# Kernel optimization log

Measured on AMD Instinct MI355X. Metric: run time of the kernel, lower is better.

The kernel has to match this reference:

```python
import jax, jax.numpy as jnp
import numpy as np

N = 10000      # num nodes
R = 16         # num relations
NB = 30        # num bases (hardcoded in source: num_bases=30)
E = 160000     # num edges
IN, HID, OUT = 256, 256, 128


def rgcn_conv(x, src, dst, etype, basis, comp, root, bias):
    """PyG RGCNConv with basis decomposition, aggr='mean' (per relation), root weight + bias."""
    # relation weights from basis decomposition: W_r = sum_b comp[r,b] * basis[b]
    W = jnp.einsum('rb,bio->rio', comp, basis)            # [R, in, out]
    xw = jnp.einsum('ni,rio->rno', x, W)                  # [R, N, out]
    msg = xw[etype, src]                                  # [E, out] gather per edge
    # per-(dst, relation) mean aggregation, then sum over relations
    seg = dst * R + etype                                 # combined segment key
    cnt = jax.ops.segment_sum(jnp.ones((msg.shape[0],), msg.dtype), seg, num_segments=N * R)
    msg = msg / jnp.maximum(cnt[seg], 1.0)[:, None]       # zero-degree -> 0 (matches scatter-mean)
    agg = jax.ops.segment_sum(msg, dst, num_segments=N)   # [N, out]
    return agg + x @ root + bias


def setup_inputs() -> dict:
    key = jax.random.key(0)
    ks = jax.random.split(key, 11)
    g = lambda k, shape, s: jax.random.normal(k, shape, jnp.float32) * s
    s1 = (2.0 / (IN + HID)) ** 0.5
    s2 = (2.0 / (HID + OUT)) ** 0.5
    return dict(
        x=g(ks[0], (N, IN), 1.0),
        edge_index=jax.random.randint(ks[1], (2, E), 0, N),
        edge_type=jax.random.randint(ks[2], (E,), 0, R),
        basis1=g(ks[3], (NB, IN, HID), s1),
        comp1=g(ks[4], (R, NB), 1.0 / NB ** 0.5),
        root1=g(ks[5], (IN, HID), s1),
        bias1=jnp.zeros((HID,), jnp.float32),
        basis2=g(ks[6], (NB, HID, OUT), s2),
        comp2=g(ks[7], (R, NB), 1.0 / NB ** 0.5),
        root2=g(ks[8], (HID, OUT), s2),
        bias2=jnp.zeros((OUT,), jnp.float32),
    )


def reference(x, edge_index, edge_type, basis1, comp1, root1, bias1,
              basis2, comp2, root2, bias2):
    src, dst = edge_index[0], edge_index[1]
    h = jax.nn.relu(rgcn_conv(x, src, dst, edge_type, basis1, comp1, root1, bias1))
    return rgcn_conv(h, src, dst, edge_type, basis2, comp2, root2, bias2)
```

## Files before the change

### kernel.cpp

```cpp
#include <hip/hip_runtime.h>
#include <hip/hip_bf16.h>

#define NN 10000
#define MP 10112
#define RR 16
#define NBASE 30
#define EE 160000
#define HIDF 256
#define OUTF 128
#define NSEG (NN * RR)

typedef __attribute__((ext_vector_type(8))) short bf16x8;
typedef __attribute__((ext_vector_type(4))) short s16x4;
typedef __attribute__((ext_vector_type(4))) float f32x4;

static __device__ __forceinline__ short f2bf(float f) {
    union { float f; unsigned u; } v; v.f = f;
    unsigned r = v.u + 0x7FFFu + ((v.u >> 16) & 1u);
    return (short)(r >> 16);
}
static __device__ __forceinline__ float bf2f(short s) {
    union { unsigned u; float f; } v;
    v.u = ((unsigned)(unsigned short)s) << 16;
    return v.f;
}
static __device__ __forceinline__ void gl16(const short* g, short* l) {
    __builtin_amdgcn_global_load_lds((const __attribute__((address_space(1))) void*)g,
                                     (__attribute__((address_space(3))) void*)l, 16, 0, 0);
}

template <int OUT>
__global__ void wtr_k(const float* __restrict__ basis, const float* __restrict__ comp,
                      const float* __restrict__ root, short* __restrict__ WT) {
    __shared__ short t[32][34];
    const int i0 = blockIdx.x * 32, n0 = blockIdx.y * 32;
    const int r = n0 / OUT, o0 = n0 % OUT;
    const int tx = threadIdx.x & 31, ty = threadIdx.x >> 5;
    #pragma unroll
    for (int dy = 0; dy < 32; dy += 8) {
        const int i = i0 + ty + dy, o = o0 + tx;
        float v;
        if (r < RR) {
            float s = 0.f;
            #pragma unroll
            for (int b = 0; b < NBASE; b++)
                s += comp[r * NBASE + b] * basis[((long)b * 256 + i) * OUT + o];
            v = s;
        } else {
            v = root[(long)i * OUT + o];
        }
        t[ty + dy][tx] = f2bf(v);
    }
    __syncthreads();
    #pragma unroll
    for (int dy = 0; dy < 32; dy += 8)
        WT[(long)(n0 + ty + dy) * 256 + i0 + tx] = t[tx][ty + dy];
}

__global__ void count_k(const int* __restrict__ dst, const int* __restrict__ et,
                        int* __restrict__ cnt) {
    int e = blockIdx.x * 256 + threadIdx.x;
    if (e < EE) atomicAdd(&cnt[dst[e] * RR + et[e]], 1);
}

__global__ void scan1_k(const int* __restrict__ cnt, int* __restrict__ incl,
                        int* __restrict__ bsum) {
    __shared__ int s[256];
    int i = blockIdx.x * 256 + threadIdx.x;
    int v = (i < NSEG) ? cnt[i] : 0;
    s[threadIdx.x] = v;
    __syncthreads();
    for (int off = 1; off < 256; off <<= 1) {
        int u = (threadIdx.x >= off) ? s[threadIdx.x - off] : 0;
        __syncthreads();
        s[threadIdx.x] += u;
        __syncthreads();
    }
    if (i < NSEG) incl[i] = s[threadIdx.x];
    if (threadIdx.x == 255) bsum[blockIdx.x] = s[255];
}

__global__ void scan2_k(int* __restrict__ bsum, int nb) {
    __shared__ int s[1024];
    int t = threadIdx.x;
    s[t] = (t < nb) ? bsum[t] : 0;
    __syncthreads();
    for (int off = 1; off < 1024; off <<= 1) {
        int u = (t >= off) ? s[t - off] : 0;
        __syncthreads();
        s[t] += u;
        __syncthreads();
    }
    if (t < nb) bsum[t] = s[t];
}

__global__ void scan3_k(const int* __restrict__ cnt, const int* __restrict__ incl,
                        const int* __restrict__ bsum, int* __restrict__ row_ptr,
                        int* __restrict__ fillpos, float* __restrict__ invc) {
    int i = blockIdx.x * 256 + threadIdx.x;
    if (i >= NSEG) return;
    int c = cnt[i];
    int off = (blockIdx.x > 0) ? bsum[blockIdx.x - 1] : 0;
    int ex = off + incl[i] - c;
    row_ptr[i] = ex;
    fillpos[i] = ex;
    invc[i] = 1.f / (float)max(c, 1);
    if (i == 0) row_ptr[NSEG] = EE;
}

__global__ void fill_k(const int* __restrict__ src, const int* __restrict__ dst,
                       const int* __restrict__ et, int* __restrict__ fillpos,
                       const float* __restrict__ invc,
                       int* __restrict__ eoff1, int* __restrict__ eoff2,
                       float* __restrict__ wgt) {
    int e = blockIdx.x * 256 + threadIdx.x;
    if (e < EE) {
        int s = src[e], t = et[e];
        int seg = dst[e] * RR + t;
        int p = atomicAdd(&fillpos[seg], 1);
        eoff1[p] = s * (17 * HIDF) + t * HIDF;
        eoff2[p] = s * (17 * OUTF) + t * OUTF;
        wgt[p] = invc[seg];
    }
}

__global__ void cvtbf_k(const float* __restrict__ X, short* __restrict__ Y) {
    int i = blockIdx.x * 256 + threadIdx.x;
    if (i >= NN * 64) return;
    float4 v = *(const float4*)(X + (long)i * 4);
    s16x4 pk = { f2bf(v.x), f2bf(v.y), f2bf(v.z), f2bf(v.w) };
    *(s16x4*)&Y[(long)i * 4] = pk;
}

template <int NTOT>
__global__ __launch_bounds__(256, 6) void gemm_xw_k(const short* __restrict__ A,
                                                    const short* __restrict__ WT,
                                                    short* __restrict__ XW) {
    constexpr int NBN = NTOT / 64;
    __shared__ __align__(16) short smem[12288];

    const int nwg = gridDim.x;
    const int q = nwg >> 3, r = nwg & 7;
    const int orig = blockIdx.x;
    const int xcd = orig & 7, wi = orig >> 3;
    const int wgid = (xcd < r ? xcd * (q + 1) : r * (q + 1) + (xcd - r) * q) + wi;
    const int m0 = (wgid / NBN) * 128;
    const int n0 = (wgid % NBN) * 64;

    const int tid = threadIdx.x;
    const int lane = tid & 63;
    const int w = tid >> 6;
    const int wr = w >> 1, wc = w & 1;
    const int al = lane & 15;
    const int cl = lane >> 4;

    int gsrcA[4];
    #pragma unroll
    for (int i = 0; i < 4; i++) {
        int ci = i * 256 + tid;
        int row = ci >> 3;
        gsrcA[i] = row * 256 + (((ci & 7) ^ (row & 7)) << 3);
    }
    int gsrcB[2];
    #pragma unroll
    for (int i = 0; i < 2; i++) {
        int ci = i * 256 + tid;
        int row = ci >> 3;
        gsrcB[i] = row * 256 + (((ci & 7) ^ (row & 7)) << 3);
    }

    int aoff[4][2], boff[2][2];
    #pragma unroll
    for (int f = 0; f < 4; f++)
        #pragma unroll
        for (int k2 = 0; k2 < 2; k2++) {
            int ra = wr * 64 + f * 16 + al;
            aoff[f][k2] = (ra << 6) + ((((k2 << 2) | cl) ^ (ra & 7)) << 3);
        }
    #pragma unroll
    for (int f = 0; f < 2; f++)
        #pragma unroll
        for (int k2 = 0; k2 < 2; k2++) {
            int rb = wc * 32 + f * 16 + al;
            boff[f][k2] = (rb << 6) + ((((k2 << 2) | cl) ^ (rb & 7)) << 3);
        }

    f32x4 acc[4][2] = {};
    const short* abase = A + (long)m0 * 256;
    const short* bbase = WT + (long)n0 * 256;

    #pragma unroll
    for (int kk = 0; kk < 256; kk += 64) {
        #pragma unroll
        for (int i = 0; i < 4; i++)
            gl16(abase + kk + gsrcA[i], &smem[i * 2048 + w * 512]);
        #pragma unroll
        for (int i = 0; i < 2; i++)
            gl16(bbase + kk + gsrcB[i], &smem[8192 + i * 2048 + w * 512]);
        __syncthreads();

        bf16x8 a[4][2], b[2][2];
        #pragma unroll
        for (int f = 0; f < 4; f++)
            #pragma unroll
            for (int k2 = 0; k2 < 2; k2++)
                a[f][k2] = *(const bf16x8*)&smem[aoff[f][k2]];
        #pragma unroll
        for (int f = 0; f < 2; f++)
            #pragma unroll
            for (int k2 = 0; k2 < 2; k2++)
                b[f][k2] = *(const bf16x8*)&smem[8192 + boff[f][k2]];
        #pragma unroll
        for (int k2 = 0; k2 < 2; k2++)
            #pragma unroll
            for (int fm = 0; fm < 4; fm++)
                #pragma unroll
                for (int fn = 0; fn < 2; fn++)
                    acc[fm][fn] = __builtin_amdgcn_mfma_f32_16x16x32_bf16(
                        a[fm][k2], b[fn][k2], acc[fm][fn], 0, 0, 0);
        __syncthreads();
    }

    #pragma unroll
    for (int fm = 0; fm < 4; fm++) {
        const int rowb = wr * 64 + fm * 16 + (cl << 2);
        #pragma unroll
        for (int fn = 0; fn < 2; fn++) {
            const int col = wc * 32 + fn * 16 + al;
            #pragma unroll
            for (int j = 0; j < 4; j++)
                smem[(rowb + j) * 68 + col] = f2bf(acc[fm][fn][j]);
        }
    }
    __syncthreads();

    #pragma unroll
    for (int pass = 0; pass < 4; pass++) {
        int c = pass * 256 + tid;
        int row = c >> 3, qq = c & 7;
        uint4 v = *(const uint4*)&smem[row * 68 + qq * 8];
        *(uint4*)&XW[(long)(m0 + row) * NTOT + n0 + qq * 8] = v;
    }
}

template <int OUT, bool L1>
__global__ void aggh_k(const int* __restrict__ rowp, const int* __restrict__ eoff,
                       const float* __restrict__ wgt, const short* __restrict__ XW,
                       const float* __restrict__ bias, short* __restrict__ Hout,
                       float* __restrict__ Fout) {
    constexpr int NTOT = 17 * OUT;
    const int n = (blockIdx.x * 256 + threadIdx.x) >> 6;
    const int lane = threadIdx.x & 63;
    if (n >= NN) return;
    const int b = rowp[n * 16], e = rowp[n * 16 + 16];

    if (L1) {
        float a0 = 0.f, a1 = 0.f, a2 = 0.f, a3 = 0.f;
        int j = b;
        for (; j + 3 < e; j += 4) {
            s16x4 v0 = *(const s16x4*)&XW[(long)eoff[j] + lane * 4];
            s16x4 v1 = *(const s16x4*)&XW[(long)eoff[j + 1] + lane * 4];
            s16x4 v2 = *(const s16x4*)&XW[(long)eoff[j + 2] + lane * 4];
            s16x4 v3 = *(const s16x4*)&XW[(long)eoff[j + 3] + lane * 4];
            float w0 = wgt[j], w1 = wgt[j + 1], w2 = wgt[j + 2], w3 = wgt[j + 3];
            a0 += w0 * bf2f(v0.x) + w1 * bf2f(v1.x) + w2 * bf2f(v2.x) + w3 * bf2f(v3.x);
            a1 += w0 * bf2f(v0.y) + w1 * bf2f(v1.y) + w2 * bf2f(v2.y) + w3 * bf2f(v3.y);
            a2 += w0 * bf2f(v0.z) + w1 * bf2f(v1.z) + w2 * bf2f(v2.z) + w3 * bf2f(v3.z);
            a3 += w0 * bf2f(v0.w) + w1 * bf2f(v1.w) + w2 * bf2f(v2.w) + w3 * bf2f(v3.w);
        }
        for (; j < e; j++) {
            int o0 = eoff[j]; float w0 = wgt[j];
            s16x4 v0 = *(const s16x4*)&XW[(long)o0 + lane * 4];
            a0 += w0 * bf2f(v0.x); a1 += w0 * bf2f(v0.y);
            a2 += w0 * bf2f(v0.z); a3 += w0 * bf2f(v0.w);
        }
        s16x4 rt = *(const s16x4*)&XW[(long)n * NTOT + 16 * OUT + lane * 4];
        f32x4 bb = *(const f32x4*)&bias[lane * 4];
        a0 = fmaxf(a0 + bf2f(rt.x) + bb.x, 0.f);
        a1 = fmaxf(a1 + bf2f(rt.y) + bb.y, 0.f);
        a2 = fmaxf(a2 + bf2f(rt.z) + bb.z, 0.f);
        a3 = fmaxf(a3 + bf2f(rt.w) + bb.w, 0.f);
        s16x4 pk = { f2bf(a0), f2bf(a1), f2bf(a2), f2bf(a3) };
        *(s16x4*)&Hout[(long)n * OUT + lane * 4] = pk;
    } else {
        float a0 = 0.f, a1 = 0.f;
        int j = b;
        for (; j + 3 < e; j += 4) {
            unsigned v0 = *(const unsigned*)&XW[(long)eoff[j] + lane * 2];
            unsigned v1 = *(const unsigned*)&XW[(long)eoff[j + 1] + lane * 2];
            unsigned v2 = *(const unsigned*)&XW[(long)eoff[j + 2] + lane * 2];
            unsigned v3 = *(const unsigned*)&XW[(long)eoff[j + 3] + lane * 2];
            float w0 = wgt[j], w1 = wgt[j + 1], w2 = wgt[j + 2], w3 = wgt[j + 3];
            a0 += w0 * bf2f((short)(v0 & 0xffff)) + w1 * bf2f((short)(v1 & 0xffff))
                + w2 * bf2f((short)(v2 & 0xffff)) + w3 * bf2f((short)(v3 & 0xffff));
            a1 += w0 * bf2f((short)(v0 >> 16)) + w1 * bf2f((short)(v1 >> 16))
                + w2 * bf2f((short)(v2 >> 16)) + w3 * bf2f((short)(v3 >> 16));
        }
        for (; j < e; j++) {
            int o0 = eoff[j]; float w0 = wgt[j];
            unsigned v0 = *(const unsigned*)&XW[(long)o0 + lane * 2];
            a0 += w0 * bf2f((short)(v0 & 0xffff));
            a1 += w0 * bf2f((short)(v0 >> 16));
        }
        unsigned rt = *(const unsigned*)&XW[(long)n * NTOT + 16 * OUT + lane * 2];
        a0 += bf2f((short)(rt & 0xffff)) + bias[lane * 2];
        a1 += bf2f((short)(rt >> 16)) + bias[lane * 2 + 1];
        float2 st = { a0, a1 };
        *(float2*)&Fout[(long)n * OUT + lane * 2] = st;
    }
}

extern "C" void kernel_launch(void* const* d_in, const int* in_sizes, int n_in,
                              void* d_out, int out_size, void* d_ws, size_t ws_size,
                              hipStream_t stream) {
    const float* x      = (const float*)d_in[0];
    const int*   ei     = (const int*)d_in[1];
    const int*   et     = (const int*)d_in[2];
    const float* basis1 = (const float*)d_in[3];
    const float* comp1  = (const float*)d_in[4];
    const float* root1  = (const float*)d_in[5];
    const float* bias1  = (const float*)d_in[6];
    const float* basis2 = (const float*)d_in[7];
    const float* comp2  = (const float*)d_in[8];
    const float* root2  = (const float*)d_in[9];
    const float* bias2  = (const float*)d_in[10];
    const int* src = ei;
    const int* dst = ei + EE;

    char* p = (char*)d_ws;
    auto take = [&](size_t bytes) { char* q = p; p += (bytes + 255) & ~(size_t)255; return q; };
    short* XW    = (short*)take((size_t)MP * 17 * HIDF * 2);
    short* WT1   = (short*)take((size_t)17 * HIDF * 256 * 2);
    short* WT2   = (short*)take((size_t)17 * OUTF * 256 * 2);
    short* Xbf   = (short*)take((size_t)MP * 256 * 2);
    short* Hbf   = (short*)take((size_t)MP * 256 * 2);
    int*   cnt   = (int*)take((size_t)NSEG * 4);
    float* invc  = (float*)take((size_t)NSEG * 4);
    int*   incl  = (int*)take((size_t)NSEG * 4);
    int*   rowp  = (int*)take((size_t)(NSEG + 1) * 4);
    int*   fpos  = (int*)take((size_t)NSEG * 4);
    int*   bsum  = (int*)take(1024 * 4);
    int*   eoff1 = (int*)take((size_t)EE * 4);
    int*   eoff2 = (int*)take((size_t)EE * 4);
    float* wgt   = (float*)take((size_t)EE * 4);

    const int NB1 = (NSEG + 255) / 256;

    hipMemsetAsync(cnt, 0, (size_t)NSEG * 4, stream);

    {
        dim3 g1(256 / 32, 17 * HIDF / 32), g2(256 / 32, 17 * OUTF / 32);
        wtr_k<HIDF><<<g1, 256, 0, stream>>>(basis1, comp1, root1, WT1);
        wtr_k<OUTF><<<g2, 256, 0, stream>>>(basis2, comp2, root2, WT2);
    }

    count_k<<<(EE + 255) / 256, 256, 0, stream>>>(dst, et, cnt);
    scan1_k<<<NB1, 256, 0, stream>>>(cnt, incl, bsum);
    scan2_k<<<1, 1024, 0, stream>>>(bsum, NB1);
    scan3_k<<<NB1, 256, 0, stream>>>(cnt, incl, bsum, rowp, fpos, invc);
    fill_k<<<(EE + 255) / 256, 256, 0, stream>>>(src, dst, et, fpos, invc, eoff1, eoff2, wgt);

    cvtbf_k<<<(NN * 64 + 255) / 256, 256, 0, stream>>>(x, Xbf);

    gemm_xw_k<17 * HIDF><<<(MP / 128) * (17 * HIDF / 64), 256, 0, stream>>>(Xbf, WT1, XW);
    aggh_k<HIDF, true><<<(NN * 64) / 256, 256, 0, stream>>>(rowp, eoff1, wgt, XW, bias1, Hbf, nullptr);

    gemm_xw_k<17 * OUTF><<<(MP / 128) * (17 * OUTF / 64), 256, 0, stream>>>(Hbf, WT2, XW);
    aggh_k<OUTF, false><<<(NN * 64) / 256, 256, 0, stream>>>(rowp, eoff2, wgt, XW, bias2, nullptr, (float*)d_out);
}
```

Baseline: 134.9 us.

## Build per-node CSR instead of per-segment CSR and fuse count with bf16 conversion

The edge CSR is now keyed by destination node only (10k rows) rather than node×relation segments (160k rows), so the scans run over far fewer elements. Per-edge mean weights are computed directly from the segment counts in the fill kernel instead of from a separate inverse-count array. The edge counting is merged with the x-to-bf16 conversion into one launch, and the memset is replaced by a zeroing kernel. This cuts launches and scan traffic in the preprocessing chain, at the cost of a second atomic per edge for the degree count.

```diff
diff --git a/kernel.cpp b/kernel.cpp
--- a/kernel.cpp
+++ b/kernel.cpp
@@ -29,6 +29,11 @@
                                      (__attribute__((address_space(3))) void*)l, 16, 0, 0);
 }
 
+__global__ void zero_k(int* __restrict__ p, int n4) {
+    int i = blockIdx.x * 256 + threadIdx.x;
+    if (i < n4) ((int4*)p)[i] = make_int4(0, 0, 0, 0);
+}
+
 template <int OUT>
 __global__ void wtr_k(const float* __restrict__ basis, const float* __restrict__ comp,
                       const float* __restrict__ root, short* __restrict__ WT) {
@@ -57,17 +62,30 @@
         WT[(long)(n0 + ty + dy) * 256 + i0 + tx] = t[tx][ty + dy];
 }
 
-__global__ void count_k(const int* __restrict__ dst, const int* __restrict__ et,
-                        int* __restrict__ cnt) {
-    int e = blockIdx.x * 256 + threadIdx.x;
-    if (e < EE) atomicAdd(&cnt[dst[e] * RR + et[e]], 1);
-}
-
-__global__ void scan1_k(const int* __restrict__ cnt, int* __restrict__ incl,
+__global__ void count_cvt_k(const float* __restrict__ X, short* __restrict__ Y,
+                            const int* __restrict__ dst, const int* __restrict__ et,
+                            int* __restrict__ cnt, int* __restrict__ deg) {
+    int b = blockIdx.x;
+    if (b < 2500) {
+        int i = b * 256 + threadIdx.x;
+        float4 v = *(const float4*)(X + (long)i * 4);
+        s16x4 pk = { f2bf(v.x), f2bf(v.y), f2bf(v.z), f2bf(v.w) };
+        *(s16x4*)&Y[(long)i * 4] = pk;
+    } else {
+        int e = (b - 2500) * 256 + threadIdx.x;
+        if (e < EE) {
+            int d = dst[e];
+            atomicAdd(&cnt[d * RR + et[e]], 1);
+            atomicAdd(&deg[d], 1);
+        }
+    }
+}
+
+__global__ void scan1_k(const int* __restrict__ deg, int* __restrict__ incl,
                         int* __restrict__ bsum) {
     __shared__ int s[256];
     int i = blockIdx.x * 256 + threadIdx.x;
-    int v = (i < NSEG) ? cnt[i] : 0;
+    int v = (i < NN) ? deg[i] : 0;
     s[threadIdx.x] = v;
     __syncthreads();
     for (int off = 1; off < 256; off <<= 1) {
@@ -76,7 +94,7 @@
         s[threadIdx.x] += u;
         __syncthreads();
     }
-    if (i < NSEG) incl[i] = s[threadIdx.x];
+    if (i < NN) incl[i] = s[threadIdx.x];
     if (threadIdx.x == 255) bsum[blockIdx.x] = s[255];
 }
 
@@ -94,42 +112,31 @@
     if (t < nb) bsum[t] = s[t];
 }
 
-__global__ void scan3_k(const int* __restrict__ cnt, const int* __restrict__ incl,
-                        const int* __restrict__ bsum, int* __restrict__ row_ptr,
-                        int* __restrict__ fillpos, float* __restrict__ invc) {
+__global__ void scan3_k(const int* __restrict__ deg, const int* __restrict__ incl,
+                        const int* __restrict__ bsum, int* __restrict__ rowp,
+                        int* __restrict__ fillpos) {
     int i = blockIdx.x * 256 + threadIdx.x;
-    if (i >= NSEG) return;
-    int c = cnt[i];
+    if (i >= NN) return;
     int off = (blockIdx.x > 0) ? bsum[blockIdx.x - 1] : 0;
-    int ex = off + incl[i] - c;
-    row_ptr[i] = ex;
+    int ex = off + incl[i] - deg[i];
+    rowp[i] = ex;
     fillpos[i] = ex;
-    invc[i] = 1.f / (float)max(c, 1);
-    if (i == 0) row_ptr[NSEG] = EE;
+    if (i == 0) rowp[NN] = EE;
 }
 
 __global__ void fill_k(const int* __restrict__ src, const int* __restrict__ dst,
                        const int* __restrict__ et, int* __restrict__ fillpos,
-                       const float* __restrict__ invc,
+                       const int* __restrict__ cnt,
                        int* __restrict__ eoff1, int* __restrict__ eoff2,
                        float* __restrict__ wgt) {
     int e = blockIdx.x * 256 + threadIdx.x;
     if (e < EE) {
-        int s = src[e], t = et[e];
-        int seg = dst[e] * RR + t;
-        int p = atomicAdd(&fillpos[seg], 1);
+        int s = src[e], t = et[e], d = dst[e];
+        int p = atomicAdd(&fillpos[d], 1);
         eoff1[p] = s * (17 * HIDF) + t * HIDF;
         eoff2[p] = s * (17 * OUTF) + t * OUTF;
-        wgt[p] = invc[seg];
-    }
-}
-
-__global__ void cvtbf_k(const float* __restrict__ X, short* __restrict__ Y) {
-    int i = blockIdx.x * 256 + threadIdx.x;
-    if (i >= NN * 64) return;
-    float4 v = *(const float4*)(X + (long)i * 4);
-    s16x4 pk = { f2bf(v.x), f2bf(v.y), f2bf(v.z), f2bf(v.w) };
-    *(s16x4*)&Y[(long)i * 4] = pk;
+        wgt[p] = 1.0f / (float)cnt[d * RR + t];
+    }
 }
 
 template <int NTOT>
@@ -252,7 +259,7 @@
     const int n = (blockIdx.x * 256 + threadIdx.x) >> 6;
     const int lane = threadIdx.x & 63;
     if (n >= NN) return;
-    const int b = rowp[n * 16], e = rowp[n * 16 + 16];
+    const int b = rowp[n], e = rowp[n + 1];
 
     if (L1) {
         float a0 = 0.f, a1 = 0.f, a2 = 0.f, a3 = 0.f;
@@ -334,19 +341,17 @@
     short* WT2   = (short*)take((size_t)17 * OUTF * 256 * 2);
     short* Xbf   = (short*)take((size_t)MP * 256 * 2);
     short* Hbf   = (short*)take((size_t)MP * 256 * 2);
-    int*   cnt   = (int*)take((size_t)NSEG * 4);
-    float* invc  = (float*)take((size_t)NSEG * 4);
-    int*   incl  = (int*)take((size_t)NSEG * 4);
-    int*   rowp  = (int*)take((size_t)(NSEG + 1) * 4);
-    int*   fpos  = (int*)take((size_t)NSEG * 4);
+    int*   cnt   = (int*)take((size_t)(NSEG + NN) * 4);
+    int*   deg   = cnt + NSEG;
+    int*   incl  = (int*)take((size_t)NN * 4);
+    int*   rowp  = (int*)take((size_t)(NN + 1) * 4);
+    int*   fpos  = (int*)take((size_t)NN * 4);
     int*   bsum  = (int*)take(1024 * 4);
     int*   eoff1 = (int*)take((size_t)EE * 4);
     int*   eoff2 = (int*)take((size_t)EE * 4);
     float* wgt   = (float*)take((size_t)EE * 4);
 
-    const int NB1 = (NSEG + 255) / 256;
-
-    hipMemsetAsync(cnt, 0, (size_t)NSEG * 4, stream);
+    zero_k<<<((NSEG + NN) / 4 + 255) / 256, 256, 0, stream>>>(cnt, (NSEG + NN) / 4);
 
     {
         dim3 g1(256 / 32, 17 * HIDF / 32), g2(256 / 32, 17 * OUTF / 32);
@@ -354,13 +359,11 @@
         wtr_k<OUTF><<<g2, 256, 0, stream>>>(basis2, comp2, root2, WT2);
     }
 
-    count_k<<<(EE + 255) / 256, 256, 0, stream>>>(dst, et, cnt);
-    scan1_k<<<NB1, 256, 0, stream>>>(cnt, incl, bsum);
-    scan2_k<<<1, 1024, 0, stream>>>(bsum, NB1);
-    scan3_k<<<NB1, 256, 0, stream>>>(cnt, incl, bsum, rowp, fpos, invc);
-    fill_k<<<(EE + 255) / 256, 256, 0, stream>>>(src, dst, et, fpos, invc, eoff1, eoff2, wgt);
-
-    cvtbf_k<<<(NN * 64 + 255) / 256, 256, 0, stream>>>(x, Xbf);
+    count_cvt_k<<<2500 + (EE + 255) / 256, 256, 0, stream>>>(x, Xbf, dst, et, cnt, deg);
+    scan1_k<<<(NN + 255) / 256, 256, 0, stream>>>(deg, incl, bsum);
+    scan2_k<<<1, 1024, 0, stream>>>(bsum, (NN + 255) / 256);
+    scan3_k<<<(NN + 255) / 256, 256, 0, stream>>>(deg, incl, bsum, rowp, fpos);
+    fill_k<<<(EE + 255) / 256, 256, 0, stream>>>(src, dst, et, fpos, cnt, eoff1, eoff2, wgt);
 
     gemm_xw_k<17 * HIDF><<<(MP / 128) * (17 * HIDF / 64), 256, 0, stream>>>(Xbf, WT1, XW);
     aggh_k<HIDF, true><<<(NN * 64) / 256, 256, 0, stream>>>(rowp, eoff1, wgt, XW, bias1, Hbf, nullptr);
```

Result: slower. 146.3 us (+8.4%).
